# Performance work log

Measured on AMD Instinct MI355X. Metric: run time of the kernel, lower is better.

The kernel has to match this reference:

```python
import jax, jax.numpy as jnp
import numpy as np

BATCH = 4096
M = 50        # CEM candidates per state
N_TOP = 32    # elites
ITERS = 100   # sequential CEM iterations
HIDDEN = 100


def setup_inputs() -> dict:
    key = jax.random.key(0)
    ks = jax.random.split(key, 7)
    states = jax.random.normal(ks[0], (BATCH, 2), dtype=jnp.float32)
    W1 = jax.random.normal(ks[1], (3, HIDDEN), dtype=jnp.float32) * 0.1
    b1 = jnp.zeros((HIDDEN,), dtype=jnp.float32)
    W2 = jax.random.normal(ks[2], (HIDDEN, HIDDEN), dtype=jnp.float32) * 0.1
    b2 = jnp.zeros((HIDDEN,), dtype=jnp.float32)
    W3 = jax.random.normal(ks[3], (HIDDEN, 1), dtype=jnp.float32) * 0.1
    b3 = jnp.zeros((1,), dtype=jnp.float32)
    return {"states": states, "W1": W1, "b1": b1, "W2": W2, "b2": b2, "W3": W3, "b3": b3}


def reference(states, W1, b1, W2, b2, W3, b3):
    batch = states.shape[0]
    states_bm = jnp.broadcast_to(states[:, None, :], (batch, M, 2))

    def qnet(angles):  # angles: (batch, M) -> q: (batch, M)
        x = jnp.concatenate([states_bm, angles[..., None]], axis=-1)  # (batch, M, 3)
        h = jax.nn.relu(x @ W1 + b1)
        h = jax.nn.relu(h @ W2 + b2)
        return (h @ W3 + b3)[..., 0]

    key = jax.random.key(42)
    k0, kloop = jax.random.split(key)
    # iteration 0: uniform random angles in [0, 1)
    angles0 = jax.random.uniform(k0, (batch, M), dtype=jnp.float32)
    q0 = qnet(angles0)

    def step(q, k):
        # NOTE: faithful to source — elites/mu/std are over Q-VALUES, and
        # new "angles" are sampled from Normal(mu_q, std_q).
        top = jax.lax.top_k(q, N_TOP)[0]                 # (batch, N_TOP)
        mu = top.mean(-1)                                # (batch,)
        std = top.std(-1, ddof=1)                        # torch unbiased std
        eps = jax.random.normal(k, (batch, M), dtype=jnp.float32)
        angles = mu[:, None] + std[:, None] * eps        # reparameterized normal
        return qnet(angles), mu

    keys = jax.random.split(kloop, ITERS - 1)
    _, mus = jax.lax.scan(step, q0, keys)
    return mus[-1] * (2.0 * jnp.pi)
```

## Files before the change

kernel.cpp:

```cpp
#include <hip/hip_runtime.h>
#include <math.h>
#include <stdint.h>

#define BATCH 4096
#define MCAND 50
#define NTOP 32
#define HID 100
#define TFL 20200

#define MINVC  (-0x1.fffffep-1f)
#define SQRT2C (0x1.6a09e6p+0f)

__device__ __forceinline__ uint32_t rotl32(uint32_t v, int d){ return (v<<d)|(v>>(32-d)); }

__device__ __forceinline__ void tf2x32(uint32_t k0, uint32_t k1, uint32_t x0, uint32_t x1,
                                       uint32_t &o0, uint32_t &o1){
  uint32_t k2 = k0 ^ k1 ^ 0x1BD11BDAu;
  x0 += k0; x1 += k1;
#define RND(r) { x0 += x1; x1 = rotl32(x1,(r)); x1 ^= x0; }
  RND(13) RND(15) RND(26) RND(6)
  x0 += k1; x1 += k2 + 1u;
  RND(17) RND(29) RND(16) RND(24)
  x0 += k2; x1 += k0 + 2u;
  RND(13) RND(15) RND(26) RND(6)
  x0 += k0; x1 += k1 + 3u;
  RND(17) RND(29) RND(16) RND(24)
  x0 += k1; x1 += k2 + 4u;
  RND(13) RND(15) RND(26) RND(6)
  x0 += k2; x1 += k0 + 5u;
#undef RND
  o0 = x0; o1 = x1;
}

__device__ __forceinline__ float erfinv32(float x){
  float w = -log1pf(-x*x);
  float p;
  if (w < 5.0f){
    w = w - 2.5f;
    p = 2.81022636e-08f;
    p = fmaf(p, w, 3.43273939e-07f);
    p = fmaf(p, w, -3.5233877e-06f);
    p = fmaf(p, w, -4.39150654e-06f);
    p = fmaf(p, w, 0.00021858087f);
    p = fmaf(p, w, -0.00125372503f);
    p = fmaf(p, w, -0.00417768164f);
    p = fmaf(p, w, 0.246640727f);
    p = fmaf(p, w, 1.50140941f);
  } else {
    w = sqrtf(w) - 3.0f;
    p = -0.000200214257f;
    p = fmaf(p, w, 0.000100950558f);
    p = fmaf(p, w, 0.00134934322f);
    p = fmaf(p, w, -0.00367342844f);
    p = fmaf(p, w, 0.00573950773f);
    p = fmaf(p, w, -0.0076224613f);
    p = fmaf(p, w, 0.00943887047f);
    p = fmaf(p, w, 1.00167406f);
    p = fmaf(p, w, 2.83297682f);
  }
  return p*x;
}

#define DPPF(v, CTRL) __int_as_float(__builtin_amdgcn_update_dpp( \
    0, __float_as_int(v), (CTRL), 0xF, 0xF, true))
#define DPPI(v, CTRL) __builtin_amdgcn_update_dpp(0, (v), (CTRL), 0xF, 0xF, true)
#define DPPADD(v, CTRL) ((v) + DPPF((v), (CTRL)))

__device__ __forceinline__ float fswap4(float v){
  float a = DPPF(v, 0x114);
  float b = DPPF(v, 0x104);
  return (threadIdx.x & 4) ? a : b;
}
__device__ __forceinline__ int iswap4(int v){
  int a = DPPI(v, 0x114), b = DPPI(v, 0x104);
  return (threadIdx.x & 4) ? a : b;
}
__device__ __forceinline__ float fswap8(float v){
  return DPPF(v, 0x128);
}
__device__ __forceinline__ float fswap16(float v){
#if __has_builtin(__builtin_amdgcn_permlane16_swap)
  auto r = __builtin_amdgcn_permlane16_swap(__float_as_uint(v), __float_as_uint(v), false, false);
  return __uint_as_float((threadIdx.x & 16) ? r[0] : r[1]);
#else
  return __shfl_xor(v, 16, 64);
#endif
}
__device__ __forceinline__ float fswap32(float v){
#if __has_builtin(__builtin_amdgcn_permlane32_swap)
  auto r = __builtin_amdgcn_permlane32_swap(__float_as_uint(v), __float_as_uint(v), false, false);
  return __uint_as_float((threadIdx.x & 32) ? r[0] : r[1]);
#else
  return __shfl_xor(v, 32, 64);
#endif
}

__global__ __launch_bounds__(512) void cem_kernel(
    const float* __restrict__ states, const float* __restrict__ W1,
    const float* __restrict__ b1,     const float* __restrict__ W2,
    const float* __restrict__ b2,     const float* __restrict__ W3,
    const float* __restrict__ b3,     float* __restrict__ out)
{
  __shared__ __align__(16) float smem[20300];
  float*  const Tb   = smem;
  float2* const T2D  = (float2*)Tb;
  int*    const ORD  = (int*)(Tb + 300);
  float*  const STm  = Tb + 400;
  float*  const AQ   = smem + 20200;
  float*  const EPB  = smem + 20250;

  const int tid  = threadIdx.x;
  const int b    = blockIdx.x;
  const int wv   = tid >> 6;
  const int lane = tid & 63;
  const int gc   = tid >> 3;
  const int gj   = tid & 7;
  const bool gact = (tid < 8*MCAND);

  float w3r[13];
#pragma unroll
  for (int i = 0; i < 13; ++i){
    int n = gj + (i<<3);
    w3r[i] = (n < HID) ? W3[n] : 0.0f;
  }
  const float sB3v = b3[0];

  uint32_t A1k = 0u, B1k = 0u, kk0 = 0u, kk1 = 0u;

  if (tid < HID){
    float u = fmaf(states[2*b], W1[tid], fmaf(states[2*b+1], W1[HID+tid], b1[tid]));
    float v = W1[2*HID+tid];
    float tt = (v != 0.0f) ? (-u / v) : INFINITY;
    Tb[tid]     = u;
    Tb[HID+tid] = v;
    Tb[200+tid] = tt;
  }
  if (tid >= 128 && tid < 128 + MCAND){
    int c = tid - 128;
    uint32_t A0, B0, a1t, b1t;
    tf2x32(0u,42u,0u,2u,A0,a1t);
    tf2x32(0u,42u,1u,3u,B0,b1t);
    uint32_t gidx = (uint32_t)b*MCAND + (uint32_t)c;
    uint32_t r0,r1,bits;
    if (gidx < 102400u){ tf2x32(A0,B0,gidx,gidx+102400u,r0,r1); bits = r0; }
    else               { tf2x32(A0,B0,gidx-102400u,gidx,r0,r1); bits = r1; }
    AQ[c] = __uint_as_float((bits>>9) | 0x3f800000u) - 1.0f;
  }
  if (wv == 7){
    uint32_t A0, B0;
    tf2x32(0u,42u,0u,2u,A0,A1k);
    tf2x32(0u,42u,1u,3u,B0,B1k);
    { uint32_t i0 = 0u; uint32_t x,y; tf2x32(A1k,B1k, i0, 99u+i0, x, y); kk0 = x; }
    { uint32_t i1 = 1u; uint32_t x,y; tf2x32(A1k,B1k, i1, 99u+i1, x, y); kk1 = x; }
  }
  __syncthreads();

  if (tid < HID){
    float tk = Tb[200+tid];
    int rk = 0;
    for (int j2 = 0; j2 < HID; ++j2){
      float tj = Tb[200+j2];
      rk += (tj < tk || (tj == tk && j2 < tid)) ? 1 : 0;
    }
    float u = Tb[tid], v = Tb[HID+tid];
    int neg = (v < 0.0f || (v == 0.0f && u > 0.0f)) ? 1 : 0;
    STm[rk] = tk;
    ORD[rk] = tid | (neg << 7);
  }
  __syncthreads();

  int kpA = 0, kpB = 0; float cuA = 0.f, cvA = 0.f, cuB = 0.f, cvB = 0.f;
  if (wv == 0){
    kpA = ORD[lane];
    int kiA = kpA & 127;
    float uA = Tb[kiA], vA = Tb[HID+kiA];
    cuA = (kpA & 128) ? -uA : uA;
    cvA = (kpA & 128) ? -vA : vA;
    if (lane < 36){
      kpB = ORD[64+lane];
      int kiB = kpB & 127;
      float uB = Tb[kiB], vB = Tb[HID+kiB];
      cuB = (kpB & 128) ? -uB : uB;
      cvB = (kpB & 128) ? -vB : vB;
    }
  }
  float st_r[13];
#pragma unroll
  for (int i = 0; i < 13; ++i){
    int idx = gj*13 + i;
    st_r[i] = (idx < HID) ? STm[idx] : INFINITY;
  }
  __syncthreads();

  if (wv == 0){
    const int L = lane;
    float a10 = b2[L], a20 = 0.0f;
    float a11 = (L < 36) ? b2[64+L] : 0.0f, a21 = 0.0f;
#pragma unroll 8
    for (int rr = 0; rr < 64; ++rr){
      int   kp = __builtin_amdgcn_readlane(kpA, rr);
      float cu = __int_as_float(__builtin_amdgcn_readlane(__float_as_int(cuA), rr));
      float cv = __int_as_float(__builtin_amdgcn_readlane(__float_as_int(cvA), rr));
      int k = kp & 127;
      float bu = (kp & 128) ? -cu : 0.0f;
      float bv = (kp & 128) ? -cv : 0.0f;
      float w0 = W2[k*HID + L];
      a10 = fmaf(bu, w0, a10); a20 = fmaf(bv, w0, a20);
      if (L < 36){
        float w1 = W2[k*HID + 64+L];
        a11 = fmaf(bu, w1, a11); a21 = fmaf(bv, w1, a21);
      }
    }
#pragma unroll 6
    for (int rr = 0; rr < 36; ++rr){
      int   kp = __builtin_amdgcn_readlane(kpB, rr);
      float cu = __int_as_float(__builtin_amdgcn_readlane(__float_as_int(cuB), rr));
      float cv = __int_as_float(__builtin_amdgcn_readlane(__float_as_int(cvB), rr));
      int k = kp & 127;
      float bu = (kp & 128) ? -cu : 0.0f;
      float bv = (kp & 128) ? -cv : 0.0f;
      float w0 = W2[k*HID + L];
      a10 = fmaf(bu, w0, a10); a20 = fmaf(bv, w0, a20);
      if (L < 36){
        float w1 = W2[k*HID + 64+L];
        a11 = fmaf(bu, w1, a11); a21 = fmaf(bv, w1, a21);
      }
    }
    { float2 f; f.x = a10; f.y = a20; T2D[L] = f; }
    if (L < 36){ float2 f; f.x = a11; f.y = a21; T2D[64+L] = f; }
#pragma unroll 8
    for (int rr = 0; rr < 64; ++rr){
      int   kp = __builtin_amdgcn_readlane(kpA, rr);
      float cu = __int_as_float(__builtin_amdgcn_readlane(__float_as_int(cuA), rr));
      float cv = __int_as_float(__builtin_amdgcn_readlane(__float_as_int(cvA), rr));
      int k = kp & 127;
      float w0 = W2[k*HID + L];
      a10 = fmaf(cu, w0, a10); a20 = fmaf(cv, w0, a20);
      { float2 f; f.x = a10; f.y = a20; T2D[(rr+1)*HID + L] = f; }
      if (L < 36){
        float w1 = W2[k*HID + 64+L];
        a11 = fmaf(cu, w1, a11); a21 = fmaf(cv, w1, a21);
        float2 f; f.x = a11; f.y = a21; T2D[(rr+1)*HID + 64+L] = f;
      }
    }
#pragma unroll 6
    for (int rr = 0; rr < 36; ++rr){
      int   kp = __builtin_amdgcn_readlane(kpB, rr);
      float cu = __int_as_float(__builtin_amdgcn_readlane(__float_as_int(cuB), rr));
      float cv = __int_as_float(__builtin_amdgcn_readlane(__float_as_int(cvB), rr));
      int k = kp & 127;
      float w0 = W2[k*HID + L];
      a10 = fmaf(cu, w0, a10); a20 = fmaf(cv, w0, a20);
      { float2 f; f.x = a10; f.y = a20; T2D[(65+rr)*HID + L] = f; }
      if (L < 36){
        float w1 = W2[k*HID + 64+L];
        a11 = fmaf(cu, w1, a11); a21 = fmaf(cv, w1, a21);
        float2 f; f.x = a11; f.y = a21; T2D[(65+rr)*HID + 64+L] = f;
      }
    }
  }
  __syncthreads();

#pragma unroll 1
  for (int t = 0; t < 99; ++t){
    if (gact){
      const float av = AQ[gc];
      int rk = 0;
#pragma unroll
      for (int i = 0; i < 13; ++i) rk += (st_r[i] < av) ? 1 : 0;
      rk += DPPI(rk, 0xB1);
      rk += DPPI(rk, 0x4E);
      rk += iswap4(rk);
      const float2* __restrict__ Trow = T2D + rk*HID;
      float acc = 0.0f;
#pragma unroll
      for (int i = 0; i < 13; ++i){
        int n = gj + (i<<3);
        n = (n < HID) ? n : gj;
        float2 tv = Trow[n];
        float h = fmaxf(fmaf(av, tv.y, tv.x), 0.0f);
        acc = fmaf(h, w3r[i], acc);
      }
      acc = DPPADD(acc, 0xB1);
      acc = DPPADD(acc, 0x4E);
      acc += fswap4(acc);
      if (gj == 0) AQ[gc] = acc;
    }
    if (wv == 7 && t < 98 && lane < MCAND){
      uint32_t gidx = (uint32_t)b*MCAND + (uint32_t)lane;
      uint32_t r0, r1, bits;
      if (gidx < 102400u){ tf2x32(kk0,kk1,gidx,gidx+102400u,r0,r1); bits = r0; }
      else               { tf2x32(kk0,kk1,gidx-102400u,gidx,r0,r1); bits = r1; }
      float fl = __uint_as_float((bits>>9) | 0x3f800000u) - 1.0f;
      float u  = fmaxf(MINVC, fl*2.0f + MINVC);
      EPB[lane] = SQRT2C * erfinv32(u);
    }
    __syncthreads();

    if (wv == 0){
      float q = (lane < MCAND) ? (AQ[lane] + sB3v) : -INFINITY;
      float v = q;
#define BST(KK, JJ, PV) { float pv = (PV); bool lower = (lane & (JJ)) == 0; \
        bool asc = (lane & (KK)) != 0; float mn = fminf(v, pv), mx = fmaxf(v, pv); \
        v = (lower == asc) ? mn : mx; }
      BST(2, 1,  DPPF(v, 0xB1))
      BST(4, 2,  DPPF(v, 0x4E))
      BST(4, 1,  DPPF(v, 0xB1))
      BST(8, 4,  fswap4(v))
      BST(8, 2,  DPPF(v, 0x4E))
      BST(8, 1,  DPPF(v, 0xB1))
      BST(16, 8, fswap8(v))
      BST(16, 4, fswap4(v))
      BST(16, 2, DPPF(v, 0x4E))
      BST(16, 1, DPPF(v, 0xB1))
      BST(32, 16, fswap16(v))
      BST(32, 8,  fswap8(v))
      BST(32, 4,  fswap4(v))
      BST(32, 2,  DPPF(v, 0x4E))
      BST(32, 1,  DPPF(v, 0xB1))
#undef BST
      {
        float pv = fswap32(v);
        v = ((lane & 32) == 0) ? fmaxf(v, pv) : fminf(v, pv);
      }
      float sv = (lane < NTOP) ? v : 0.0f;
      sv += fswap32(sv);
      sv += fswap16(sv);
      sv += fswap8(sv);
      sv += fswap4(sv);
      sv = DPPADD(sv, 0x4E);
      sv = DPPADD(sv, 0xB1);
      float mun = sv / 32.0f;
      float dv = (lane < NTOP) ? (v - mun) : 0.0f;
      float s2 = dv*dv;
      s2 += fswap32(s2);
      s2 += fswap16(s2);
      s2 += fswap8(s2);
      s2 += fswap4(s2);
      s2 = DPPADD(s2, 0x4E);
      s2 = DPPADD(s2, 0xB1);
      float stdv = sqrtf(s2 / 31.0f);
      if (t == 98){
        if (lane == 0) out[b] = mun * 6.2831854820251465f;
      } else if (lane < MCAND){
        AQ[lane] = fmaf(stdv, EPB[lane], mun);
      }
    } else if (wv == 7 && t < 98){
      uint32_t nt = (uint32_t)(t + 1);
      { uint32_t i0 = 2u*nt;      uint32_t ii = (i0 < 99u) ? i0 : (i0 - 99u);
        uint32_t x,y; tf2x32(A1k,B1k, ii, 99u+ii, x, y); kk0 = (i0 < 99u) ? x : y; }
      { uint32_t i1 = 2u*nt + 1u; uint32_t ii = (i1 < 99u) ? i1 : (i1 - 99u);
        uint32_t x,y; tf2x32(A1k,B1k, ii, 99u+ii, x, y); kk1 = (i1 < 99u) ? x : y; }
    }
    __syncthreads();
  }
}

extern "C" void kernel_launch(void* const* d_in, const int* in_sizes, int n_in,
                              void* d_out, int out_size, void* d_ws, size_t ws_size,
                              hipStream_t stream) {
  const float* states = (const float*)d_in[0];
  const float* W1     = (const float*)d_in[1];
  const float* b1     = (const float*)d_in[2];
  const float* W2     = (const float*)d_in[3];
  const float* b2     = (const float*)d_in[4];
  const float* W3     = (const float*)d_in[5];
  const float* b3     = (const float*)d_in[6];
  float* out = (float*)d_out;
  hipLaunchKernelGGL(cem_kernel, dim3(BATCH), dim3(512), 0, stream,
                     states, W1, b1, W2, b2, W3, b3, out);
}
```

Measured before the change: 1.383 ms.

## Precompute all CEM noise in a separate parallel kernel into workspace

```diff
diff --git a/kernel.cpp b/kernel.cpp
--- a/kernel.cpp
+++ b/kernel.cpp
@@ -7,6 +7,9 @@
 #define NTOP 32
 #define HID 100
 #define TFL 20200
+#define EPS_ROWS 98
+#define EPS_ROWSZ (BATCH*MCAND)
+#define WS_NEED   (1024u + (size_t)EPS_ROWS*EPS_ROWSZ*4u)
 
 #define MINVC  (-0x1.fffffep-1f)
 #define SQRT2C (0x1.6a09e6p+0f)
@@ -95,11 +98,45 @@
 #endif
 }
 
+__global__ void keys_kernel(uint32_t* __restrict__ K){
+  int tid = threadIdx.x;
+  if (tid < 99){
+    uint32_t A0, B0, A1, B1;
+    tf2x32(0u,42u,0u,2u,A0,A1);
+    tf2x32(0u,42u,1u,3u,B0,B1);
+    (void)A0; (void)B0;
+    uint32_t o0,o1;
+    tf2x32(A1,B1,(uint32_t)tid,(uint32_t)(99+tid),o0,o1);
+    K[tid]    = o0;
+    K[99+tid] = o1;
+  }
+}
+
+__device__ __forceinline__ float bits2norm(uint32_t bits){
+  float fl = __uint_as_float((bits>>9) | 0x3f800000u) - 1.0f;
+  float u  = fmaxf(MINVC, fl*2.0f + MINVC);
+  return SQRT2C * erfinv32(u);
+}
+
+__global__ __launch_bounds__(256) void eps_kernel(const uint32_t* __restrict__ K,
+                                                  float* __restrict__ E){
+  int id = blockIdx.x*256 + threadIdx.x;
+  int t  = id / 102400;
+  int g  = id - t*102400;
+  uint32_t kk0 = K[2*t], kk1 = K[2*t+1];
+  uint32_t r0, r1;
+  tf2x32(kk0,kk1,(uint32_t)g,(uint32_t)g+102400u,r0,r1);
+  E[(size_t)t*EPS_ROWSZ + g]           = bits2norm(r0);
+  E[(size_t)t*EPS_ROWSZ + g + 102400]  = bits2norm(r1);
+}
+
+template<bool EPSG>
 __global__ __launch_bounds__(512) void cem_kernel(
     const float* __restrict__ states, const float* __restrict__ W1,
     const float* __restrict__ b1,     const float* __restrict__ W2,
     const float* __restrict__ b2,     const float* __restrict__ W3,
-    const float* __restrict__ b3,     float* __restrict__ out)
+    const float* __restrict__ b3,     const float* __restrict__ epsg,
+    float* __restrict__ out)
 {
   __shared__ __align__(16) float smem[20300];
   float*  const Tb   = smem;
@@ -146,7 +183,7 @@
     else               { tf2x32(A0,B0,gidx-102400u,gidx,r0,r1); bits = r1; }
     AQ[c] = __uint_as_float((bits>>9) | 0x3f800000u) - 1.0f;
   }
-  if (wv == 7){
+  if (!EPSG && wv == 7){
     uint32_t A0, B0;
     tf2x32(0u,42u,0u,2u,A0,A1k);
     tf2x32(0u,42u,1u,3u,B0,B1k);
@@ -271,29 +308,33 @@
       rk += DPPI(rk, 0xB1);
       rk += DPPI(rk, 0x4E);
       rk += iswap4(rk);
-      const float2* __restrict__ Trow = T2D + rk*HID;
+      const char* rowp = (const char*)T2D + (((rk*HID) + gj) << 3);
       float acc = 0.0f;
 #pragma unroll
-      for (int i = 0; i < 13; ++i){
-        int n = gj + (i<<3);
-        n = (n < HID) ? n : gj;
-        float2 tv = Trow[n];
+      for (int i = 0; i < 12; ++i){
+        float2 tv = *(const float2*)(rowp + (i << 6));
         float h = fmaxf(fmaf(av, tv.y, tv.x), 0.0f);
         acc = fmaf(h, w3r[i], acc);
+      }
+      if (gj < 4){
+        float2 tv = *(const float2*)(rowp + (12 << 6));
+        float h = fmaxf(fmaf(av, tv.y, tv.x), 0.0f);
+        acc = fmaf(h, w3r[12], acc);
       }
       acc = DPPADD(acc, 0xB1);
       acc = DPPADD(acc, 0x4E);
       acc += fswap4(acc);
       if (gj == 0) AQ[gc] = acc;
     }
-    if (wv == 7 && t < 98 && lane < MCAND){
+    if (EPSG){
+      if (wv == 7 && t < EPS_ROWS && lane < MCAND)
+        EPB[lane] = epsg[(size_t)t*EPS_ROWSZ + (size_t)b*MCAND + (size_t)lane];
+    } else if (wv == 7 && t < EPS_ROWS && lane < MCAND){
       uint32_t gidx = (uint32_t)b*MCAND + (uint32_t)lane;
       uint32_t r0, r1, bits;
       if (gidx < 102400u){ tf2x32(kk0,kk1,gidx,gidx+102400u,r0,r1); bits = r0; }
       else               { tf2x32(kk0,kk1,gidx-102400u,gidx,r0,r1); bits = r1; }
-      float fl = __uint_as_float((bits>>9) | 0x3f800000u) - 1.0f;
-      float u  = fmaxf(MINVC, fl*2.0f + MINVC);
-      EPB[lane] = SQRT2C * erfinv32(u);
+      EPB[lane] = bits2norm(bits);
     }
     __syncthreads();
 
@@ -345,7 +386,7 @@
       } else if (lane < MCAND){
         AQ[lane] = fmaf(stdv, EPB[lane], mun);
       }
-    } else if (wv == 7 && t < 98){
+    } else if (!EPSG && wv == 7 && t < EPS_ROWS){
       uint32_t nt = (uint32_t)(t + 1);
       { uint32_t i0 = 2u*nt;      uint32_t ii = (i0 < 99u) ? i0 : (i0 - 99u);
         uint32_t x,y; tf2x32(A1k,B1k, ii, 99u+ii, x, y); kk0 = (i0 < 99u) ? x : y; }
@@ -367,6 +408,16 @@
   const float* W3     = (const float*)d_in[5];
   const float* b3     = (const float*)d_in[6];
   float* out = (float*)d_out;
-  hipLaunchKernelGGL(cem_kernel, dim3(BATCH), dim3(512), 0, stream,
-                     states, W1, b1, W2, b2, W3, b3, out);
-}
+
+  if (d_ws != nullptr && ws_size >= WS_NEED){
+    uint32_t* K = (uint32_t*)d_ws;
+    float*    E = (float*)((char*)d_ws + 1024);
+    hipLaunchKernelGGL(keys_kernel, dim3(1), dim3(128), 0, stream, K);
+    hipLaunchKernelGGL(eps_kernel, dim3(EPS_ROWS*102400/256), dim3(256), 0, stream, K, E);
+    hipLaunchKernelGGL(HIP_KERNEL_NAME(cem_kernel<true>), dim3(BATCH), dim3(512), 0, stream,
+                       states, W1, b1, W2, b2, W3, b3, (const float*)E, out);
+  } else {
+    hipLaunchKernelGGL(HIP_KERNEL_NAME(cem_kernel<false>), dim3(BATCH), dim3(512), 0, stream,
+                       states, W1, b1, W2, b2, W3, b3, (const float*)nullptr, out);
+  }
+}
```

Measured after the change: 1.316 ms. 4.9% less time.
